# Kernel optimization log

Hardware: AMD Instinct MI355X
Metric: run time of the kernel (lower is better)

The kernel has to match this reference:

```python
import jax, jax.numpy as jnp
import numpy as np
import math

B, S, D = 2, 1024, 1024
H, KVH = 16, 4
HD = D // H            # 64
WIN = 256              # sliding window size
E, TOPK = 8, 2
DFF = 4096
T = B * S
CAP = max(1, int(1.0 * T / E))   # capacity_factor=1.0 -> 256
EPS = 1e-6
NEG_INF = float('-inf')


def setup_inputs() -> dict:
    key = jax.random.key(0)
    ks = jax.random.split(key, 10)
    x = jax.random.normal(ks[0], (B, S, D), dtype=jnp.float32)
    # causal additive mask (B,1,S,S)
    i = jnp.arange(S)[:, None]
    j = jnp.arange(S)[None, :]
    causal = jnp.where(j <= i, 0.0, NEG_INF).astype(jnp.float32)
    mask = jnp.broadcast_to(causal[None, None], (B, 1, S, S))
    global_token_mask = jax.random.uniform(ks[1], (B, S)) < 0.05
    sd = 1.0 / math.sqrt(D)
    Wq = jax.random.normal(ks[2], (D, D), jnp.float32) * sd
    Wk = jax.random.normal(ks[3], (D, D), jnp.float32) * sd
    Wv = jax.random.normal(ks[4], (D, D), jnp.float32) * sd
    Wo = jax.random.normal(ks[5], (D, D), jnp.float32) * sd
    g1 = jnp.ones((D,), jnp.float32)
    g2 = jnp.ones((D,), jnp.float32)
    Wgate = jax.random.normal(ks[6], (D, E), jnp.float32) * 0.02
    W1 = jax.random.normal(ks[7], (E, D, 2 * DFF), jnp.float32) * sd
    W2 = jax.random.normal(ks[8], (E, DFF, D), jnp.float32) * (1.0 / math.sqrt(DFF))
    return {"x": x, "mask": mask, "global_token_mask": global_token_mask,
            "Wq": Wq, "Wk": Wk, "Wv": Wv, "Wo": Wo,
            "g1": g1, "g2": g2, "Wgate": Wgate, "W1": W1, "W2": W2}


def _rope_tables():
    inv_freq = 1.0 / (10000.0 ** (jnp.arange(0, HD, 2, dtype=jnp.float32) / HD))
    t = jnp.arange(S, dtype=jnp.float32)
    freqs = t[:, None] * inv_freq[None, :]          # (S, HD/2)
    emb = jnp.concatenate([freqs, freqs], axis=-1)  # (S, HD)
    return emb[None, None].astype(jnp.float32), None  # placeholder


def _rotate_half(x):
    x1, x2 = jnp.split(x, 2, axis=-1)
    return jnp.concatenate([-x2, x1], axis=-1)


def _rmsnorm(x, g):
    return g * x * jax.lax.rsqrt(jnp.mean(x * x, axis=-1, keepdims=True) + EPS)


def _attention(x, mask, gtm, Wq, Wk, Wv, Wo):
    # The torch GQA view/permute chain reduces exactly to a plain head split.
    q = (x @ Wq).reshape(B, S, H, HD).transpose(0, 2, 1, 3)  # (B,H,S,HD)
    k = (x @ Wk).reshape(B, S, H, HD).transpose(0, 2, 1, 3)
    v = (x @ Wv).reshape(B, S, H, HD).transpose(0, 2, 1, 3)
    # inline RoPE
    inv_freq = 1.0 / (10000.0 ** (jnp.arange(0, HD, 2, dtype=jnp.float32) / HD))
    t = jnp.arange(S, dtype=jnp.float32)
    freqs = t[:, None] * inv_freq[None, :]
    emb = jnp.concatenate([freqs, freqs], axis=-1)  # (S,HD)
    cos = jnp.cos(emb)[None, None]
    sin = jnp.sin(emb)[None, None]
    q = q * cos + _rotate_half(q) * sin
    k = k * cos + _rotate_half(k) * sin
    scores = jnp.einsum('bhqd,bhkd->bhqk', q, k) / math.sqrt(HD)
    # sliding-window mask
    i = jnp.arange(S)[:, None]
    j = jnp.arange(S)[None, :]
    diff = i - j
    swa = jnp.where((diff < 0) | (diff >= WIN), NEG_INF, 0.0).astype(scores.dtype)
    combined = mask + swa[None, None]               # (B,1,S,S)
    gt = gtm[:, None, :, None]                      # query is global
    gs = gtm[:, None, None, :]                      # key is global
    combined = jnp.where(gt | gs, 0.0, combined)
    attn = jax.nn.softmax(scores + combined, axis=-1)
    out = jnp.einsum('bhqk,bhkd->bhqd', attn, v)
    out = out.transpose(0, 2, 1, 3).reshape(B, S, D)
    return out @ Wo


def _moe(x, Wgate, W1, W2):
    flat_x = x.reshape(T, D)
    gate_scores = jax.nn.softmax(flat_x @ Wgate, axis=-1)          # (T,E)
    topk_vals, topk_idx = jax.lax.top_k(gate_scores, TOPK)          # (T,k)
    phi_mean = jnp.mean(gate_scores, axis=0)
    aux_loss = E * jnp.sum(phi_mean * phi_mean)
    # per-token weight for each expert (0 if not routed)
    w = jnp.zeros((T, E), flat_x.dtype).at[jnp.arange(T)[:, None], topk_idx].add(topk_vals)
    # capacity: pick top-CAP tokens by weight per expert. Unrouted tokens have
    # weight 0 so any that slip in contribute exactly 0 (matches torch semantics).
    sel_w, sel_idx = jax.lax.top_k(w.T, CAP)                        # (E,CAP)
    tok = flat_x[sel_idx]                                           # (E,CAP,D)
    h = jnp.einsum('ecd,edf->ecf', tok, W1)                         # (E,CAP,2*DFF)
    h1, h2 = jnp.split(h, 2, axis=-1)
    act = h1 * jax.nn.silu(h2)                                      # SwiGLU
    out_e = jnp.einsum('ecf,efd->ecd', act, W2) * sel_w[..., None]
    combined = jnp.zeros((T, D), flat_x.dtype).at[sel_idx.reshape(-1)].add(out_e.reshape(-1, D))
    return combined.reshape(B, S, D), aux_loss


def reference(x, mask, global_token_mask, Wq, Wk, Wv, Wo, g1, g2, Wgate, W1, W2):
    # pre-norm residual block (SublayerConnection with RMSNorm, dropout=identity in eval)
    h = x + _attention(_rmsnorm(x, g1), mask, global_token_mask, Wq, Wk, Wv, Wo)
    moe_out, aux_loss = _moe(_rmsnorm(h, g2), Wgate, W1, W2)
    out = h + moe_out
    return out, aux_loss
```

## Files before the change

kernel.cpp:

```cpp
#include <hip/hip_runtime.h>
#include <hip/hip_bf16.h>
#include <math.h>

#define T_TOK 2048
#define DMODEL 1024
#define NH 16
#define HD 64
#define S_LEN 1024
#define NE 8
#define CAP 256
#define DFF 4096

typedef __attribute__((ext_vector_type(8))) short bf16x8;
typedef __attribute__((ext_vector_type(4))) float f32x4;

__device__ inline unsigned short f2bf(float f) {
    union { float f; unsigned int u; } x; x.f = f;
    unsigned int u = x.u;
    unsigned int r = (u + 0x7FFFu + ((u >> 16) & 1u)) >> 16;
    return (unsigned short)r;
}

__device__ inline float bf2f(unsigned short h) {
    union { unsigned int u; float f; } x; x.u = (unsigned int)h << 16; return x.f;
}

__device__ inline unsigned int pkbf(float lo, float hi) {
    __hip_bfloat162 h2 = __float22bfloat162_rn(make_float2(lo, hi));
    unsigned int r;
    __builtin_memcpy(&r, &h2, 4);
    return r;
}

__device__ inline void gload16(const void* g, void* l) {
    __builtin_amdgcn_global_load_lds(
        (const __attribute__((address_space(1))) unsigned int*)g,
        (__attribute__((address_space(3))) unsigned int*)l, 16, 0, 0);
}

__global__ void rope_table_kernel(float* __restrict__ rc, float* __restrict__ rs,
                                  float* __restrict__ gsum) {
    int s = blockIdx.x;
    int i = threadIdx.x;
    float invf = powf(10000.0f, -(float)(2 * i) / 64.0f);
    float ang = (float)s * invf;
    rc[s * 32 + i] = cosf(ang);
    rs[s * 32 + i] = sinf(ang);
    if (blockIdx.x == 0 && threadIdx.x < 8) gsum[threadIdx.x] = 0.f;
}

template <int OUTBF>
__global__ __launch_bounds__(256) void rmsnorm_kernel(const float* __restrict__ x,
                                                      const float* __restrict__ g,
                                                      void* __restrict__ yv) {
    __shared__ float red[256];
    int t = blockIdx.x;
    int tid = threadIdx.x;
    const float* xr = x + (size_t)t * DMODEL;
    float ss = 0.f;
    for (int d = tid; d < DMODEL; d += 256) { float v = xr[d]; ss += v * v; }
    red[tid] = ss; __syncthreads();
    for (int o = 128; o > 0; o >>= 1) { if (tid < o) red[tid] += red[tid + o]; __syncthreads(); }
    float scale = 1.0f / sqrtf(red[0] / (float)DMODEL + 1e-6f);
    if (OUTBF) {
        unsigned short* yr = (unsigned short*)yv + (size_t)t * DMODEL;
        for (int d = tid; d < DMODEL; d += 256) yr[d] = f2bf(g[d] * xr[d] * scale);
    } else {
        float* yr = (float*)yv + (size_t)t * DMODEL;
        for (int d = tid; d < DMODEL; d += 256) yr[d] = g[d] * xr[d] * scale;
    }
}

__global__ __launch_bounds__(256) void gemm_qkv_rope(const unsigned short* __restrict__ xn,
                                                     const float* __restrict__ Wq,
                                                     const float* __restrict__ Wk,
                                                     const float* __restrict__ Wv,
                                                     const float* __restrict__ rc,
                                                     const float* __restrict__ rs,
                                                     unsigned short* __restrict__ Qh,
                                                     unsigned short* __restrict__ Ql,
                                                     unsigned short* __restrict__ Kh,
                                                     unsigned short* __restrict__ Kl,
                                                     unsigned short* __restrict__ Vtb) {
    __shared__ unsigned short As[128 * 64];
    __shared__ unsigned int Bp[64 * 32];
    const int mat = blockIdx.x >> 4;
    const int h = blockIdx.x & 15;
    const float* B = ((mat == 0) ? Wq : (mat == 1) ? Wk : Wv) + h * 64;
    const int by = blockIdx.y * 128;
    const int tid = threadIdx.x, l = tid & 63, wid = tid >> 6;
    const int g = l >> 4;
    const int kp = tid >> 3;
    const int nc = tid & 7;
    const int chunk = kp >> 2, within = kp & 3;

    f32x4 acc[2][4] = {};

    for (int k0 = 0; k0 < 1024; k0 += 64) {
        #pragma unroll
        for (int i = 0; i < 4; i++) {
            int c = i * 256 + tid;
            int row = c >> 3, sl = c & 7, gs = sl ^ (row & 7);
            gload16(xn + (size_t)(by + row) * 1024 + k0 + gs * 8, &As[c * 8]);
        }
        const float* Brow = B + (size_t)(k0 + 2 * kp) * 1024 + nc * 8;
        float4 a0 = *(const float4*)(Brow);
        float4 a1 = *(const float4*)(Brow + 4);
        float4 b0 = *(const float4*)(Brow + 1024);
        float4 b1 = *(const float4*)(Brow + 1028);
        unsigned int p[8];
        p[0] = pkbf(a0.x, b0.x); p[1] = pkbf(a0.y, b0.y);
        p[2] = pkbf(a0.z, b0.z); p[3] = pkbf(a0.w, b0.w);
        p[4] = pkbf(a1.x, b1.x); p[5] = pkbf(a1.y, b1.y);
        p[6] = pkbf(a1.z, b1.z); p[7] = pkbf(a1.w, b1.w);
        #pragma unroll
        for (int i = 0; i < 8; i++) {
            int n_loc = nc * 8 + i;
            int idx = n_loc * 32 + ((chunk ^ (n_loc & 7)) << 2) + within;
            Bp[idx] = p[i];
        }
        __syncthreads();
        #pragma unroll
        for (int ks = 0; ks < 2; ks++) {
            bf16x8 af[2];
            #pragma unroll
            for (int m = 0; m < 2; m++) {
                int row = wid * 32 + m * 16 + (l & 15);
                int sl = (ks * 4 + g) ^ (row & 7);
                af[m] = *(const bf16x8*)&As[row * 64 + sl * 8];
            }
            #pragma unroll
            for (int nf = 0; nf < 4; nf++) {
                int n_loc = nf * 16 + (l & 15);
                int base = n_loc * 32 + (((ks * 4 + g) ^ (n_loc & 7)) << 2);
                bf16x8 bfr = *(const bf16x8*)&Bp[base];
                #pragma unroll
                for (int m = 0; m < 2; m++)
                    acc[m][nf] = __builtin_amdgcn_mfma_f32_16x16x32_bf16(af[m], bfr, acc[m][nf], 0, 0, 0);
            }
        }
        __syncthreads();
    }

    if (mat < 2) {
        unsigned short* Dh = (mat == 0) ? Qh : Kh;
        unsigned short* Dl = (mat == 0) ? Ql : Kl;
        float scale = (mat == 0) ? 0.125f : 1.0f;
        #pragma unroll
        for (int m = 0; m < 2; m++)
            #pragma unroll
            for (int r = 0; r < 4; r++) {
                int t = by + wid * 32 + m * 16 + g * 4 + r;
                int b = t >> 10, s = t & 1023;
                size_t ob = ((size_t)(b * 16 + h) * 1024 + s) * 64;
                #pragma unroll
                for (int pr = 0; pr < 2; pr++) {
                    int i = pr * 16 + (l & 15);
                    float c = rc[s * 32 + i], sn = rs[s * 32 + i];
                    float a = acc[m][pr][r], bb = acc[m][pr + 2][r];
                    float v0 = (a * c - bb * sn) * scale;
                    float v1 = (bb * c + a * sn) * scale;
                    unsigned short h0 = f2bf(v0), h1 = f2bf(v1);
                    Dh[ob + i] = h0;      Dl[ob + i] = f2bf(v0 - bf2f(h0));
                    Dh[ob + i + 32] = h1; Dl[ob + i + 32] = f2bf(v1 - bf2f(h1));
                }
            }
    } else {
        #pragma unroll
        for (int m = 0; m < 2; m++) {
            int t0 = by + wid * 32 + m * 16 + g * 4;
            int b = t0 >> 10, s0 = t0 & 1023;
            #pragma unroll
            for (int nf = 0; nf < 4; nf++) {
                int d = nf * 16 + (l & 15);
                unsigned short tmp[4];
                #pragma unroll
                for (int r = 0; r < 4; r++) tmp[r] = f2bf(acc[m][nf][r]);
                *(uint2*)&Vtb[((size_t)(b * 16 + h) * 64 + d) * 1024 + s0] = *(uint2*)tmp;
            }
        }
    }
}

template <int RES>
__global__ __launch_bounds__(256) void gemm_bf32(const unsigned short* __restrict__ A,
                                                 const float* __restrict__ B,
                                                 const float* __restrict__ Rr,
                                                 float* __restrict__ C,
                                                 int K, int lda,
                                                 long long sA, long long sB, long long sC) {
    __shared__ unsigned short As[128 * 64];
    __shared__ unsigned int Bp[32 * 32];
    A += (long long)blockIdx.z * sA + (long long)blockIdx.y * 128 * lda;
    B += (long long)blockIdx.z * sB;
    C += (long long)blockIdx.z * sC + (long long)blockIdx.y * 128 * 1024;
    const float* Rp = RES ? (Rr + (long long)blockIdx.y * 128 * 1024) : nullptr;
    const int bx = blockIdx.x * 32;
    const int tid = threadIdx.x, l = tid & 63, wid = tid >> 6;
    const int g = l >> 4;
    const int kp = tid >> 3;
    const int nc = tid & 7;
    const int chunk = kp >> 2, within = kp & 3;

    f32x4 acc[2][2] = {};

    for (int k0 = 0; k0 < K; k0 += 64) {
        #pragma unroll
        for (int i = 0; i < 4; i++) {
            int c = i * 256 + tid;
            int row = c >> 3, sl = c & 7, gs = sl ^ (row & 7);
            gload16(A + (size_t)row * lda + k0 + gs * 8, &As[c * 8]);
        }
        const float* Brow = B + (size_t)(k0 + 2 * kp) * 1024 + bx + nc * 4;
        float4 a0 = *(const float4*)(Brow);
        float4 a1 = *(const float4*)(Brow + 1024);
        unsigned int p1[4];
        p1[0] = pkbf(a0.x, a1.x); p1[1] = pkbf(a0.y, a1.y);
        p1[2] = pkbf(a0.z, a1.z); p1[3] = pkbf(a0.w, a1.w);
        #pragma unroll
        for (int i = 0; i < 4; i++) {
            int n_loc = nc * 4 + i;
            int idx = n_loc * 32 + ((chunk ^ (n_loc & 7)) << 2) + within;
            Bp[idx] = p1[i];
        }
        __syncthreads();
        #pragma unroll
        for (int ks = 0; ks < 2; ks++) {
            bf16x8 af[2];
            #pragma unroll
            for (int m = 0; m < 2; m++) {
                int row = wid * 32 + m * 16 + (l & 15);
                int sl = (ks * 4 + g) ^ (row & 7);
                af[m] = *(const bf16x8*)&As[row * 64 + sl * 8];
            }
            #pragma unroll
            for (int nf = 0; nf < 2; nf++) {
                int n_loc = nf * 16 + (l & 15);
                int base = n_loc * 32 + (((ks * 4 + g) ^ (n_loc & 7)) << 2);
                bf16x8 bfr = *(const bf16x8*)&Bp[base];
                #pragma unroll
                for (int m = 0; m < 2; m++)
                    acc[m][nf] = __builtin_amdgcn_mfma_f32_16x16x32_bf16(af[m], bfr, acc[m][nf], 0, 0, 0);
            }
        }
        __syncthreads();
    }
    #pragma unroll
    for (int m = 0; m < 2; m++) {
        int row0 = wid * 32 + m * 16 + g * 4;
        #pragma unroll
        for (int nf = 0; nf < 2; nf++) {
            int col = bx + nf * 16 + (l & 15);
            #pragma unroll
            for (int r = 0; r < 4; r++) {
                size_t idx = (size_t)(row0 + r) * 1024 + col;
                float v = acc[m][nf][r];
                if (RES) v += Rp[idx];
                C[idx] = v;
            }
        }
    }
}

__global__ __launch_bounds__(256) void gemm_w1_fused(const unsigned short* __restrict__ tok,
                                                     const float* __restrict__ W1,
                                                     unsigned short* __restrict__ act) {
    __shared__ unsigned short As[256 * 64];
    __shared__ unsigned int B1p[32 * 32];
    __shared__ unsigned int B2p[32 * 32];
    const int e = blockIdx.y;
    const int bx = blockIdx.x * 32;
    const unsigned short* A = tok + (size_t)e * CAP * DMODEL;
    const float* B = W1 + (size_t)e * DMODEL * (2 * DFF);
    unsigned short* C = act + (size_t)e * CAP * DFF;
    const int tid = threadIdx.x, l = tid & 63, wid = tid >> 6;
    const int g = l >> 4;
    const int kp = tid >> 3;
    const int nc = tid & 7;
    const int chunk = kp >> 2, within = kp & 3;

    f32x4 acc1[4][2] = {};
    f32x4 acc2[4][2] = {};

    for (int k0 = 0; k0 < DMODEL; k0 += 64) {
        #pragma unroll
        for (int i = 0; i < 8; i++) {
            int c = i * 256 + tid;
            int row = c >> 3, sl = c & 7, gs = sl ^ (row & 7);
            gload16(A + (size_t)row * DMODEL + k0 + gs * 8, &As[c * 8]);
        }
        const float* Brow = B + (size_t)(k0 + 2 * kp) * 8192 + bx + nc * 4;
        float4 a0 = *(const float4*)(Brow);
        float4 a1 = *(const float4*)(Brow + 8192);
        float4 c0 = *(const float4*)(Brow + 4096);
        float4 c1 = *(const float4*)(Brow + 4096 + 8192);
        unsigned int p1[4], p2[4];
        p1[0] = pkbf(a0.x, a1.x); p1[1] = pkbf(a0.y, a1.y);
        p1[2] = pkbf(a0.z, a1.z); p1[3] = pkbf(a0.w, a1.w);
        p2[0] = pkbf(c0.x, c1.x); p2[1] = pkbf(c0.y, c1.y);
        p2[2] = pkbf(c0.z, c1.z); p2[3] = pkbf(c0.w, c1.w);
        #pragma unroll
        for (int i = 0; i < 4; i++) {
            int n_loc = nc * 4 + i;
            int idx = n_loc * 32 + ((chunk ^ (n_loc & 7)) << 2) + within;
            B1p[idx] = p1[i];
            B2p[idx] = p2[i];
        }
        __syncthreads();
        #pragma unroll
        for (int ks = 0; ks < 2; ks++) {
            bf16x8 af[4];
            #pragma unroll
            for (int m = 0; m < 4; m++) {
                int row = wid * 64 + m * 16 + (l & 15);
                int sl = (ks * 4 + g) ^ (row & 7);
                af[m] = *(const bf16x8*)&As[row * 64 + sl * 8];
            }
            #pragma unroll
            for (int nf = 0; nf < 2; nf++) {
                int n_loc = nf * 16 + (l & 15);
                int base = n_loc * 32 + (((ks * 4 + g) ^ (n_loc & 7)) << 2);
                bf16x8 b1 = *(const bf16x8*)&B1p[base];
                bf16x8 b2 = *(const bf16x8*)&B2p[base];
                #pragma unroll
                for (int m = 0; m < 4; m++) {
                    acc1[m][nf] = __builtin_amdgcn_mfma_f32_16x16x32_bf16(af[m], b1, acc1[m][nf], 0, 0, 0);
                    acc2[m][nf] = __builtin_amdgcn_mfma_f32_16x16x32_bf16(af[m], b2, acc2[m][nf], 0, 0, 0);
                }
            }
        }
        __syncthreads();
    }
    #pragma unroll
    for (int m = 0; m < 4; m++) {
        int row0 = wid * 64 + m * 16 + g * 4;
        #pragma unroll
        for (int nf = 0; nf < 2; nf++) {
            int col = bx + nf * 16 + (l & 15);
            #pragma unroll
            for (int r = 0; r < 4; r++) {
                float h1 = acc1[m][nf][r], h2 = acc2[m][nf][r];
                float sil = h2 / (1.0f + __expf(-h2));
                C[(size_t)(row0 + r) * DFF + col] = f2bf(h1 * sil);
            }
        }
    }
}

__global__ __launch_bounds__(256) void attn_mfma_kernel(const unsigned short* __restrict__ Qh,
                                                        const unsigned short* __restrict__ Ql,
                                                        const unsigned short* __restrict__ Kh,
                                                        const unsigned short* __restrict__ Kl,
                                                        const unsigned short* __restrict__ Vtb,
                                                        const int* __restrict__ gtm,
                                                        unsigned short* __restrict__ o) {
    __shared__ unsigned short Ksh[64 * 64];
    __shared__ unsigned short Ksl[64 * 64];
    __shared__ unsigned short Vs[64 * 64];
    __shared__ unsigned short Pl[4][16 * 64];
    const int qt = blockIdx.x, h = blockIdx.y, b = blockIdx.z;
    const int bh = b * 16 + h;
    const int tid = threadIdx.x, l = tid & 63, w = tid >> 6;
    const int q0 = qt * 64 + w * 16;
    const unsigned short* Qhb = Qh + (size_t)bh * 1024 * 64;
    const unsigned short* Qlb = Ql + (size_t)bh * 1024 * 64;
    const unsigned short* Khb = Kh + (size_t)bh * 1024 * 64;
    const unsigned short* Klb = Kl + (size_t)bh * 1024 * 64;
    const unsigned short* Vbh = Vtb + (size_t)bh * 64 * 1024;
    const int* gb = gtm + b * 1024;

    bf16x8 afh[2], afl[2];
    #pragma unroll
    for (int ks = 0; ks < 2; ks++) {
        size_t off = (size_t)(q0 + (l & 15)) * 64 + ks * 32 + (l >> 4) * 8;
        afh[ks] = *(const bf16x8*)(Qhb + off);
        afl[ks] = *(const bf16x8*)(Qlb + off);
    }

    int gqm = 0;
    #pragma unroll
    for (int r = 0; r < 4; r++)
        gqm |= (gb[q0 + (l >> 4) * 4 + r] ? 1 : 0) << r;

    f32x4 acc_o[4] = {};
    float m_run[4], l_run[4];
    #pragma unroll
    for (int r = 0; r < 4; r++) { m_run[r] = -1e30f; l_run[r] = 0.f; }

    for (int jt = 0; jt < 16; jt++) {
        const int j0 = jt * 64;
        #pragma unroll
        for (int i = 0; i < 2; i++) {
            int c = i * 256 + tid, row = c >> 3, sl = c & 7, gs = sl ^ (row & 7);
            gload16(Khb + (size_t)(j0 + row) * 64 + gs * 8, &Ksh[c * 8]);
            gload16(Klb + (size_t)(j0 + row) * 64 + gs * 8, &Ksl[c * 8]);
            gload16(Vbh + (size_t)row * 1024 + j0 + gs * 8, &Vs[c * 8]);
        }
        __syncthreads();

        f32x4 sv[4] = {};
        #pragma unroll
        for (int n = 0; n < 4; n++) {
            #pragma unroll
            for (int ks = 0; ks < 2; ks++) {
                int row = n * 16 + (l & 15);
                int sl = (ks * 4 + (l >> 4)) ^ (row & 7);
                bf16x8 khf = *(const bf16x8*)&Ksh[row * 64 + sl * 8];
                bf16x8 klf = *(const bf16x8*)&Ksl[row * 64 + sl * 8];
                sv[n] = __builtin_amdgcn_mfma_f32_16x16x32_bf16(afl[ks], khf, sv[n], 0, 0, 0);
                sv[n] = __builtin_amdgcn_mfma_f32_16x16x32_bf16(afh[ks], klf, sv[n], 0, 0, 0);
                sv[n] = __builtin_amdgcn_mfma_f32_16x16x32_bf16(afh[ks], khf, sv[n], 0, 0, 0);
            }
        }

        int gk[4];
        #pragma unroll
        for (int n = 0; n < 4; n++) gk[n] = gb[j0 + n * 16 + (l & 15)];

        #pragma unroll
        for (int n = 0; n < 4; n++)
            #pragma unroll
            for (int r = 0; r < 4; r++) {
                int q = q0 + (l >> 4) * 4 + r;
                int k = j0 + n * 16 + (l & 15);
                bool allowed = ((gqm >> r) & 1) || gk[n] || ((k <= q) && (q - k < 256));
                if (!allowed) sv[n][r] = -1e30f;
            }

        {
            float tm[4], corr[4], rsum[4];
            #pragma unroll
            for (int r = 0; r < 4; r++)
                tm[r] = fmaxf(fmaxf(sv[0][r], sv[1][r]), fmaxf(sv[2][r], sv[3][r]));
            #pragma unroll
            for (int wd = 1; wd <= 8; wd <<= 1)
                #pragma unroll
                for (int r = 0; r < 4; r++) tm[r] = fmaxf(tm[r], __shfl_xor(tm[r], wd, 64));
            #pragma unroll
            for (int r = 0; r < 4; r++) {
                float mn = fmaxf(m_run[r], tm[r]);
                corr[r] = __expf(m_run[r] - mn);
                m_run[r] = mn;
                rsum[r] = 0.f;
            }
            #pragma unroll
            for (int n = 0; n < 4; n++)
                #pragma unroll
                for (int r = 0; r < 4; r++) {
                    float p = __expf(sv[n][r] - m_run[r]);
                    sv[n][r] = p;
                    rsum[r] += p;
                }
            #pragma unroll
            for (int wd = 1; wd <= 8; wd <<= 1)
                #pragma unroll
                for (int r = 0; r < 4; r++) rsum[r] += __shfl_xor(rsum[r], wd, 64);
            #pragma unroll
            for (int r = 0; r < 4; r++) l_run[r] = l_run[r] * corr[r] + rsum[r];
            #pragma unroll
            for (int nd = 0; nd < 4; nd++)
                #pragma unroll
                for (int r = 0; r < 4; r++) acc_o[nd][r] *= corr[r];
            #pragma unroll
            for (int n = 0; n < 4; n++)
                #pragma unroll
                for (int r = 0; r < 4; r++) {
                    int qr = (l >> 4) * 4 + r;
                    int kc = n * 16 + (l & 15);
                    int byte = (qr * 128 + kc * 2) ^ ((qr & 7) << 4);
                    Pl[w][byte >> 1] = f2bf(sv[n][r]);
                }
        }

        asm volatile("s_waitcnt lgkmcnt(0)" ::: "memory");
        __builtin_amdgcn_sched_barrier(0);

        #pragma unroll
        for (int ks = 0; ks < 2; ks++) {
            int prow = l & 15;
            int psl = (ks * 4 + (l >> 4)) ^ (prow & 7);
            bf16x8 pa = *(const bf16x8*)&Pl[w][prow * 64 + psl * 8];
            #pragma unroll
            for (int nd = 0; nd < 4; nd++) {
                int row = nd * 16 + (l & 15);
                int sl = (ks * 4 + (l >> 4)) ^ (row & 7);
                bf16x8 vf = *(const bf16x8*)&Vs[row * 64 + sl * 8];
                acc_o[nd] = __builtin_amdgcn_mfma_f32_16x16x32_bf16(pa, vf, acc_o[nd], 0, 0, 0);
            }
        }
        __syncthreads();
    }

    #pragma unroll
    for (int r = 0; r < 4; r++) {
        float inv = 1.0f / l_run[r];
        int t_ = b * 1024 + q0 + (l >> 4) * 4 + r;
        #pragma unroll
        for (int nd = 0; nd < 4; nd++) {
            int col = h * 64 + nd * 16 + (l & 15);
            o[(size_t)t_ * 1024 + col] = f2bf(acc_o[nd][r] * inv);
        }
    }
}

__global__ __launch_bounds__(256) void gate_kernel(const float* __restrict__ hn,
                                                   const float* __restrict__ Wgate,
                                                   float* __restrict__ wfull,
                                                   int* __restrict__ slot,
                                                   float* __restrict__ gate_sum) {
    int tid = threadIdx.x;
    int w = tid >> 6, l = tid & 63;
    int t = blockIdx.x * 4 + w;
    int e = l & 7, g = l >> 3;
    const float* xr = hn + (size_t)t * DMODEL;
    const float* wp = Wgate + l;
    float acc = 0.f;
    #pragma unroll 8
    for (int kk = 0; kk < 128; kk++)
        acc += xr[g + 8 * kk] * wp[64 * kk];
    #pragma unroll
    for (int o = 8; o < 64; o <<= 1) acc += __shfl_xor(acc, o, 64);
    float m = acc;
    #pragma unroll
    for (int o = 1; o < 8; o <<= 1) m = fmaxf(m, __shfl_xor(m, o, 64));
    float p = __expf(acc - m);
    float s = p;
    #pragma unroll
    for (int o = 1; o < 8; o <<= 1) s += __shfl_xor(s, o, 64);
    float pr = p / s;
    unsigned long long key = ((unsigned long long)__float_as_uint(pr) << 32) | (unsigned)(7 - e);
    unsigned long long k1 = key;
    #pragma unroll
    for (int o = 1; o < 8; o <<= 1) { unsigned long long t2 = __shfl_xor(k1, o, 64); if (t2 > k1) k1 = t2; }
    int e1 = 7 - (int)(k1 & 7);
    unsigned long long key2 = (e == e1) ? 0ull : key;
    unsigned long long k2 = key2;
    #pragma unroll
    for (int o = 1; o < 8; o <<= 1) { unsigned long long t2 = __shfl_xor(k2, o, 64); if (t2 > k2) k2 = t2; }
    int e2 = 7 - (int)(k2 & 7);
    if (l < 8) {
        wfull[t * 8 + e] = (e == e1 || e == e2) ? pr : 0.f;
        slot[t * 8 + e] = -1;
        atomicAdd(&gate_sum[e], pr);
    }
}

__global__ __launch_bounds__(1024) void expert_select_kernel(const float* __restrict__ wfull,
                                                             float* __restrict__ sw,
                                                             int* __restrict__ sidx,
                                                             int* __restrict__ slot) {
    __shared__ unsigned long long keys[2048];
    int e = blockIdx.x;
    int t = threadIdx.x;
    for (int i = t; i < 2048; i += 1024) {
        float w = wfull[i * 8 + e];
        unsigned int wb = __float_as_uint(w);
        keys[i] = ((unsigned long long)wb << 32) | (unsigned long long)(0xFFFFFFFFu - (unsigned int)i);
    }
    __syncthreads();
    for (int k = 2; k <= 2048; k <<= 1) {
        for (int j = k >> 1; j > 0; j >>= 1) {
            for (int i = t; i < 2048; i += 1024) {
                int ixj = i ^ j;
                if (ixj > i) {
                    bool desc = ((i & k) == 0);
                    unsigned long long a = keys[i], b = keys[ixj];
                    if ((a < b) == desc) { keys[i] = b; keys[ixj] = a; }
                }
            }
            __syncthreads();
        }
    }
    if (t < CAP) {
        unsigned long long kk = keys[t];
        float w = __uint_as_float((unsigned int)(kk >> 32));
        int idx = (int)(0xFFFFFFFFu - (unsigned int)(kk & 0xFFFFFFFFu));
        sw[e * CAP + t] = w;
        sidx[e * CAP + t] = idx;
        if (w > 0.f) slot[idx * 8 + e] = t;
    }
}

__global__ __launch_bounds__(256) void gather_tok_kernel(const float* __restrict__ hn,
                                                         const int* __restrict__ sidx,
                                                         const float* __restrict__ sw,
                                                         unsigned short* __restrict__ tok) {
    int ec = blockIdx.x;
    int tid = threadIdx.x;
    float w = sw[ec];
    int src = sidx[ec];
    const float* s = hn + (size_t)src * DMODEL;
    unsigned short* d = tok + (size_t)ec * DMODEL;
    for (int i = tid; i < DMODEL; i += 256) d[i] = (w > 0.f) ? f2bf(s[i]) : 0;
}

__global__ __launch_bounds__(256) void combine_kernel(const float* __restrict__ h,
                                                      const float* __restrict__ out_e,
                                                      const int* __restrict__ slot,
                                                      const float* __restrict__ wfull,
                                                      const float* __restrict__ gate_sum,
                                                      float* __restrict__ out) {
    int t = blockIdx.x;
    int tid = threadIdx.x;
    for (int d = tid; d < DMODEL; d += 256) {
        float acc = h[(size_t)t * DMODEL + d];
        #pragma unroll
        for (int e = 0; e < 8; e++) {
            int c = slot[t * 8 + e];
            if (c >= 0) acc += wfull[t * 8 + e] * out_e[((size_t)(e * CAP + c)) * DMODEL + d];
        }
        out[(size_t)t * DMODEL + d] = acc;
    }
    if (t == 0 && tid == 0) {
        float a = 0.f;
        #pragma unroll
        for (int e = 0; e < 8; e++) { float m = gate_sum[e] / (float)T_TOK; a += m * m; }
        out[(size_t)T_TOK * DMODEL] = 8.0f * a;
    }
}

extern "C" void kernel_launch(void* const* d_in, const int* in_sizes, int n_in,
                              void* d_out, int out_size, void* d_ws, size_t ws_size,
                              hipStream_t stream) {
    const float* x     = (const float*)d_in[0];
    const int*   gtm   = (const int*)d_in[2];
    const float* Wq    = (const float*)d_in[3];
    const float* Wk    = (const float*)d_in[4];
    const float* Wv    = (const float*)d_in[5];
    const float* Wo    = (const float*)d_in[6];
    const float* g1    = (const float*)d_in[7];
    const float* g2    = (const float*)d_in[8];
    const float* Wgate = (const float*)d_in[9];
    const float* W1    = (const float*)d_in[10];
    const float* W2    = (const float*)d_in[11];
    float* out = (float*)d_out;

    char* ws = (char*)d_ws;
    unsigned short* Qh   = (unsigned short*)(ws + 0);
    unsigned short* Ql   = (unsigned short*)(ws + 4194304);
    unsigned short* Kh   = (unsigned short*)(ws + 8388608);
    unsigned short* Kl   = (unsigned short*)(ws + 12582912);
    unsigned short* Vtb  = (unsigned short*)(ws + 16777216);
    unsigned short* act  = (unsigned short*)(ws + 0);
    unsigned short* xn   = (unsigned short*)(ws + 20971520);
    unsigned short* attno= (unsigned short*)(ws + 25165824);
    float* hb    = (float*)(ws + 29360128);
    float* hnb   = (float*)(ws + 37748736);
    float* oute  = (float*)(ws + 46137344);
    unsigned short* tok = (unsigned short*)(ws + 54525952);
    float* ropec = (float*)(ws + 58720256);
    float* ropes = (float*)(ws + 58851328);
    float* wfull = (float*)(ws + 58982400);
    int*   slot  = (int*)(ws + 59047936);
    float* sw    = (float*)(ws + 59113472);
    int*   sidx  = (int*)(ws + 59121664);
    float* gsum  = (float*)(ws + 59129856);

    rope_table_kernel<<<S_LEN, 32, 0, stream>>>(ropec, ropes, gsum);
    rmsnorm_kernel<1><<<T_TOK, 256, 0, stream>>>(x, g1, xn);

    gemm_qkv_rope<<<dim3(48, 16, 1), 256, 0, stream>>>(
        xn, Wq, Wk, Wv, ropec, ropes, Qh, Ql, Kh, Kl, Vtb);

    attn_mfma_kernel<<<dim3(16, 16, 2), 256, 0, stream>>>(Qh, Ql, Kh, Kl, Vtb, gtm, attno);

    gemm_bf32<1><<<dim3(32, 16, 1), 256, 0, stream>>>(
        attno, Wo, x, hb, 1024, 1024, 0, 0, 0);
    rmsnorm_kernel<0><<<T_TOK, 256, 0, stream>>>(hb, g2, hnb);

    gate_kernel<<<T_TOK / 4, 256, 0, stream>>>(hnb, Wgate, wfull, slot, gsum);
    expert_select_kernel<<<NE, 1024, 0, stream>>>(wfull, sw, sidx, slot);
    gather_tok_kernel<<<NE * CAP, 256, 0, stream>>>(hnb, sidx, sw, tok);

    gemm_w1_fused<<<dim3(128, 8, 1), 256, 0, stream>>>(tok, W1, act);
    gemm_bf32<0><<<dim3(32, 2, 8), 256, 0, stream>>>(
        act, W2, nullptr, oute, 4096, 4096,
        (long long)CAP * DFF, (long long)DFF * 1024, (long long)CAP * 1024);

    combine_kernel<<<T_TOK, 256, 0, stream>>>(hb, oute, slot, wfull, gsum, out);
}
```

Before: 356.4 us.

## Prefetch next-tile weights in GEMMs and double-buffer K/V in attention

Result: no change. 353.5 us (-0.8%).

```diff
diff --git a/kernel.cpp b/kernel.cpp
--- a/kernel.cpp
+++ b/kernel.cpp
@@ -96,6 +96,12 @@
 
     f32x4 acc[2][4] = {};
 
+    const float* Brow = B + (size_t)(2 * kp) * 1024 + nc * 8;
+    float4 a0 = *(const float4*)(Brow);
+    float4 a1 = *(const float4*)(Brow + 4);
+    float4 b0 = *(const float4*)(Brow + 1024);
+    float4 b1 = *(const float4*)(Brow + 1028);
+
     for (int k0 = 0; k0 < 1024; k0 += 64) {
         #pragma unroll
         for (int i = 0; i < 4; i++) {
@@ -103,11 +109,6 @@
             int row = c >> 3, sl = c & 7, gs = sl ^ (row & 7);
             gload16(xn + (size_t)(by + row) * 1024 + k0 + gs * 8, &As[c * 8]);
         }
-        const float* Brow = B + (size_t)(k0 + 2 * kp) * 1024 + nc * 8;
-        float4 a0 = *(const float4*)(Brow);
-        float4 a1 = *(const float4*)(Brow + 4);
-        float4 b0 = *(const float4*)(Brow + 1024);
-        float4 b1 = *(const float4*)(Brow + 1028);
         unsigned int p[8];
         p[0] = pkbf(a0.x, b0.x); p[1] = pkbf(a0.y, b0.y);
         p[2] = pkbf(a0.z, b0.z); p[3] = pkbf(a0.w, b0.w);
@@ -120,6 +121,13 @@
             Bp[idx] = p[i];
         }
         __syncthreads();
+        if (k0 + 64 < 1024) {
+            const float* Bn = B + (size_t)(k0 + 64 + 2 * kp) * 1024 + nc * 8;
+            a0 = *(const float4*)(Bn);
+            a1 = *(const float4*)(Bn + 4);
+            b0 = *(const float4*)(Bn + 1024);
+            b1 = *(const float4*)(Bn + 1028);
+        }
         #pragma unroll
         for (int ks = 0; ks < 2; ks++) {
             bf16x8 af[2];
@@ -204,6 +212,10 @@
 
     f32x4 acc[2][2] = {};
 
+    const float* Brow = B + (size_t)(2 * kp) * 1024 + bx + nc * 4;
+    float4 a0 = *(const float4*)(Brow);
+    float4 a1 = *(const float4*)(Brow + 1024);
+
     for (int k0 = 0; k0 < K; k0 += 64) {
         #pragma unroll
         for (int i = 0; i < 4; i++) {
@@ -211,9 +223,6 @@
             int row = c >> 3, sl = c & 7, gs = sl ^ (row & 7);
             gload16(A + (size_t)row * lda + k0 + gs * 8, &As[c * 8]);
         }
-        const float* Brow = B + (size_t)(k0 + 2 * kp) * 1024 + bx + nc * 4;
-        float4 a0 = *(const float4*)(Brow);
-        float4 a1 = *(const float4*)(Brow + 1024);
         unsigned int p1[4];
         p1[0] = pkbf(a0.x, a1.x); p1[1] = pkbf(a0.y, a1.y);
         p1[2] = pkbf(a0.z, a1.z); p1[3] = pkbf(a0.w, a1.w);
@@ -224,6 +233,11 @@
             Bp[idx] = p1[i];
         }
         __syncthreads();
+        if (k0 + 64 < K) {
+            const float* Bn = B + (size_t)(k0 + 64 + 2 * kp) * 1024 + bx + nc * 4;
+            a0 = *(const float4*)(Bn);
+            a1 = *(const float4*)(Bn + 1024);
+        }
         #pragma unroll
         for (int ks = 0; ks < 2; ks++) {
             bf16x8 af[2];
@@ -282,6 +296,12 @@
     f32x4 acc1[4][2] = {};
     f32x4 acc2[4][2] = {};
 
+    const float* Brow = B + (size_t)(2 * kp) * 8192 + bx + nc * 4;
+    float4 a0 = *(const float4*)(Brow);
+    float4 a1 = *(const float4*)(Brow + 8192);
+    float4 c0 = *(const float4*)(Brow + 4096);
+    float4 c1 = *(const float4*)(Brow + 4096 + 8192);
+
     for (int k0 = 0; k0 < DMODEL; k0 += 64) {
         #pragma unroll
         for (int i = 0; i < 8; i++) {
@@ -289,11 +309,6 @@
             int row = c >> 3, sl = c & 7, gs = sl ^ (row & 7);
             gload16(A + (size_t)row * DMODEL + k0 + gs * 8, &As[c * 8]);
         }
-        const float* Brow = B + (size_t)(k0 + 2 * kp) * 8192 + bx + nc * 4;
-        float4 a0 = *(const float4*)(Brow);
-        float4 a1 = *(const float4*)(Brow + 8192);
-        float4 c0 = *(const float4*)(Brow + 4096);
-        float4 c1 = *(const float4*)(Brow + 4096 + 8192);
         unsigned int p1[4], p2[4];
         p1[0] = pkbf(a0.x, a1.x); p1[1] = pkbf(a0.y, a1.y);
         p1[2] = pkbf(a0.z, a1.z); p1[3] = pkbf(a0.w, a1.w);
@@ -307,6 +322,13 @@
             B2p[idx] = p2[i];
         }
         __syncthreads();
+        if (k0 + 64 < DMODEL) {
+            const float* Bn = B + (size_t)(k0 + 64 + 2 * kp) * 8192 + bx + nc * 4;
+            a0 = *(const float4*)(Bn);
+            a1 = *(const float4*)(Bn + 8192);
+            c0 = *(const float4*)(Bn + 4096);
+            c1 = *(const float4*)(Bn + 4096 + 8192);
+        }
         #pragma unroll
         for (int ks = 0; ks < 2; ks++) {
             bf16x8 af[4];
@@ -354,9 +376,9 @@
                                                         const unsigned short* __restrict__ Vtb,
                                                         const int* __restrict__ gtm,
                                                         unsigned short* __restrict__ o) {
-    __shared__ unsigned short Ksh[64 * 64];
-    __shared__ unsigned short Ksl[64 * 64];
-    __shared__ unsigned short Vs[64 * 64];
+    __shared__ unsigned short Ksh[2][64 * 64];
+    __shared__ unsigned short Ksl[2][64 * 64];
+    __shared__ unsigned short Vs[2][64 * 64];
     __shared__ unsigned short Pl[4][16 * 64];
     const int qt = blockIdx.x, h = blockIdx.y, b = blockIdx.z;
     const int bh = b * 16 + h;
@@ -387,31 +409,49 @@
     #pragma unroll
     for (int r = 0; r < 4; r++) { m_run[r] = -1e30f; l_run[r] = 0.f; }
 
+    {
+        #pragma unroll
+        for (int i = 0; i < 2; i++) {
+            int c = i * 256 + tid, row = c >> 3, sl = c & 7, gs = sl ^ (row & 7);
+            gload16(Khb + (size_t)row * 64 + gs * 8, &Ksh[0][c * 8]);
+            gload16(Klb + (size_t)row * 64 + gs * 8, &Ksl[0][c * 8]);
+            gload16(Vbh + (size_t)row * 1024 + gs * 8, &Vs[0][c * 8]);
+        }
+    }
+    int cur = 0;
+
     for (int jt = 0; jt < 16; jt++) {
         const int j0 = jt * 64;
-        #pragma unroll
-        for (int i = 0; i < 2; i++) {
-            int c = i * 256 + tid, row = c >> 3, sl = c & 7, gs = sl ^ (row & 7);
-            gload16(Khb + (size_t)(j0 + row) * 64 + gs * 8, &Ksh[c * 8]);
-            gload16(Klb + (size_t)(j0 + row) * 64 + gs * 8, &Ksl[c * 8]);
-            gload16(Vbh + (size_t)row * 1024 + j0 + gs * 8, &Vs[c * 8]);
-        }
         __syncthreads();
 
+        if (jt < 15) {
+            const int jn = j0 + 64;
+            int nb = cur ^ 1;
+            #pragma unroll
+            for (int i = 0; i < 2; i++) {
+                int c = i * 256 + tid, row = c >> 3, sl = c & 7, gs = sl ^ (row & 7);
+                gload16(Khb + (size_t)(jn + row) * 64 + gs * 8, &Ksh[nb][c * 8]);
+                gload16(Klb + (size_t)(jn + row) * 64 + gs * 8, &Ksl[nb][c * 8]);
+                gload16(Vbh + (size_t)row * 1024 + jn + gs * 8, &Vs[nb][c * 8]);
+            }
+        }
+
         f32x4 sv[4] = {};
+        __builtin_amdgcn_s_setprio(1);
         #pragma unroll
         for (int n = 0; n < 4; n++) {
             #pragma unroll
             for (int ks = 0; ks < 2; ks++) {
                 int row = n * 16 + (l & 15);
                 int sl = (ks * 4 + (l >> 4)) ^ (row & 7);
-                bf16x8 khf = *(const bf16x8*)&Ksh[row * 64 + sl * 8];
-                bf16x8 klf = *(const bf16x8*)&Ksl[row * 64 + sl * 8];
+                bf16x8 khf = *(const bf16x8*)&Ksh[cur][row * 64 + sl * 8];
+                bf16x8 klf = *(const bf16x8*)&Ksl[cur][row * 64 + sl * 8];
                 sv[n] = __builtin_amdgcn_mfma_f32_16x16x32_bf16(afl[ks], khf, sv[n], 0, 0, 0);
                 sv[n] = __builtin_amdgcn_mfma_f32_16x16x32_bf16(afh[ks], klf, sv[n], 0, 0, 0);
                 sv[n] = __builtin_amdgcn_mfma_f32_16x16x32_bf16(afh[ks], khf, sv[n], 0, 0, 0);
             }
         }
+        __builtin_amdgcn_s_setprio(0);
 
         int gk[4];
         #pragma unroll
@@ -475,6 +515,7 @@
         asm volatile("s_waitcnt lgkmcnt(0)" ::: "memory");
         __builtin_amdgcn_sched_barrier(0);
 
+        __builtin_amdgcn_s_setprio(1);
         #pragma unroll
         for (int ks = 0; ks < 2; ks++) {
             int prow = l & 15;
@@ -484,11 +525,12 @@
             for (int nd = 0; nd < 4; nd++) {
                 int row = nd * 16 + (l & 15);
                 int sl = (ks * 4 + (l >> 4)) ^ (row & 7);
-                bf16x8 vf = *(const bf16x8*)&Vs[row * 64 + sl * 8];
+                bf16x8 vf = *(const bf16x8*)&Vs[cur][row * 64 + sl * 8];
                 acc_o[nd] = __builtin_amdgcn_mfma_f32_16x16x32_bf16(pa, vf, acc_o[nd], 0, 0, 0);
             }
         }
-        __syncthreads();
+        __builtin_amdgcn_s_setprio(0);
+        cur ^= 1;
     }
 
     #pragma unroll
```
